# Optimization experiments

Measured on AMD Instinct MI355X. Metric: run time of the kernel, lower is better.

Reference implementation:

```python
import jax, jax.numpy as jnp
import numpy as np

TOTAL = 131072   # total frames across all utterances
SEG = 256        # number of utterances
FEAT = 78        # input feature dim (hardcoded by Linear(78,1024))
HID = 1024
NCLS = 10


def _linear_params(key, fan_in, fan_out):
    # torch nn.Linear default init: U(-1/sqrt(fan_in), 1/sqrt(fan_in))
    bound = 1.0 / np.sqrt(fan_in)
    kw, kb = jax.random.split(key)
    W = jax.random.uniform(kw, (fan_in, fan_out), minval=-bound, maxval=bound, dtype=jnp.float32)
    b = jax.random.uniform(kb, (fan_out,), minval=-bound, maxval=bound, dtype=jnp.float32)
    return W, b


def setup_inputs() -> dict:
    key = jax.random.key(0)
    ks = jax.random.split(key, 8)
    # ragged lengths summing exactly to TOTAL
    rng = np.random.default_rng(0)
    raw = rng.integers(256, 768, size=SEG).astype(np.float64)
    lens = np.maximum(1, (raw * TOTAL / raw.sum()).astype(np.int64))
    lens[-1] += TOTAL - lens.sum()
    lengths = jnp.asarray(lens, dtype=jnp.int32)

    x = jax.random.normal(ks[0], (TOTAL, FEAT), dtype=jnp.float32)
    W1, b1 = _linear_params(ks[1], FEAT, HID)
    W2, b2 = _linear_params(ks[2], HID, HID)
    W3, b3 = _linear_params(ks[3], HID, HID)
    W4, b4 = _linear_params(ks[4], HID, HID)
    W5, b5 = _linear_params(ks[5], HID, 1)
    W6, b6 = _linear_params(ks[6], HID, HID)
    W7, b7 = _linear_params(ks[7], HID, NCLS)
    return dict(x=x, W1=W1, b1=b1, W2=W2, b2=b2, W3=W3, b3=b3, W4=W4, b4=b4,
                W5=W5, b5=b5, W6=W6, b6=b6, W7=W7, b7=b7, lengths=lengths)


def reference(x, W1, b1, W2, b2, W3, b3, W4, b4, W5, b5, W6, b6, W7, b7, lengths):
    h = jax.nn.relu(x @ W1 + b1)
    h = jax.nn.relu(h @ W2 + b2)
    h = jax.nn.relu(h @ W3 + b3)
    h = jax.nn.relu(h @ W4 + b4)            # [N, HID]
    scores = jax.nn.relu(h @ W5 + b5)[:, 0]  # per-frame attention logit [N]

    # per-segment softmax over frames, then weighted sum pooling (fused segment ops)
    n_seg = lengths.shape[0]
    seg = jnp.repeat(jnp.arange(n_seg, dtype=jnp.int32), lengths,
                     total_repeat_length=h.shape[0])          # [N] segment ids
    m = jax.ops.segment_max(scores, seg, num_segments=n_seg)  # stable softmax max
    e = jnp.exp(scores - m[seg])
    denom = jax.ops.segment_sum(e, seg, num_segments=n_seg)
    w = e / denom[seg]                                        # [N] softmax weights
    pooled = jax.ops.segment_sum(h * w[:, None], seg, num_segments=n_seg)  # [SEG, HID]

    out = jax.nn.relu(pooled @ W6 + b6) @ W7 + b7             # [SEG, 10]
    return out
```

## Files before the change

### kernel.cpp

```cpp
#include <hip/hip_runtime.h>
#include <hip/hip_fp16.h>

#define TOTAL 131072
#define SEGN  256
#define FEAT  78
#define FPAD  96
#define HID   1024
#define NCLS  10
#define FCHUNK 32

typedef __attribute__((ext_vector_type(8))) short short8;
typedef __attribute__((ext_vector_type(4))) float floatx4;

typedef __attribute__((address_space(1))) void gvoid_t;
typedef __attribute__((address_space(3))) void svoid_t;

__device__ __forceinline__ void async_copy16(const void* gsrc, void* ldst) {
    __builtin_amdgcn_global_load_lds((gvoid_t*)(void*)gsrc, (svoid_t*)ldst, 16, 0, 0);
}


__global__ void conv_x_slab(const float* __restrict__ x, __half* __restrict__ xb,
                            int row0, int rows) {
    int idx = blockIdx.x * 256 + threadIdx.x;
    if (idx >= rows * FPAD) return;
    int col = idx % FPAD;
    int r   = idx / FPAD;
    float v = (col < FEAT) ? x[(size_t)(row0 + r) * FEAT + col] : 0.0f;
    xb[idx] = __float2half(v);
}

__global__ void conv_wt_kernel(const float* __restrict__ W, __half* __restrict__ Wt,
                               int K, int N, int Kpad) {
    int idx = blockIdx.x * 256 + threadIdx.x;
    if (idx >= N * Kpad) return;
    int k = idx % Kpad;
    int n = idx / Kpad;
    float v = (k < K) ? W[(size_t)k * N + n] : 0.0f;
    Wt[idx] = __float2half(v);
}

__global__ void conv_w4_kernel(const float* __restrict__ W2, const float* __restrict__ W3,
                               const float* __restrict__ W4, const float* __restrict__ W6,
                               __half* __restrict__ w2t, __half* __restrict__ w3t,
                               __half* __restrict__ w4t, __half* __restrict__ w6t) {
    int idx = blockIdx.x * 256 + threadIdx.x;
    if (idx >= HID * HID) return;
    int k = idx % HID;
    int n = idx / HID;
    const float* Ws[4] = {W2, W3, W4, W6};
    __half* Ts[4] = {w2t, w3t, w4t, w6t};
    int w = blockIdx.y;
    Ts[w][idx] = __float2half(Ws[w][(size_t)k * HID + n]);
}


__global__ __launch_bounds__(256, 2)
void gemm_f16(const __half* __restrict__ A, const __half* __restrict__ Bt,
              __half* __restrict__ C, const float* __restrict__ bias,
              int M, int N, int K, int relu_flag)
{
    __shared__ __align__(16) short smem[128 * 32 * 2];
    short* lds_a = smem;
    short* lds_b = smem + 128 * 32;

    const int t   = threadIdx.x;
    const int nbn = N >> 7;
    const int nbm = M >> 7;
    int bm, bn;
    {
        const int b = blockIdx.x;
        if ((nbm & 7) == 0) {
            const int xcd = b & 7;
            const int j   = b >> 3;
            bm = xcd * (nbm >> 3) + j / nbn;
            bn = j % nbn;
        } else {
            bn = b % nbn;
            bm = b / nbn;
        }
    }
    const size_t m0 = (size_t)bm * 128;
    const size_t n0 = (size_t)bn * 128;
    const int wave = t >> 6, lane = t & 63;
    const int wm = (wave >> 1) << 6;
    const int wn = (wave & 1) << 6;
    const int l16 = lane & 15, q = lane >> 4;

    floatx4 acc[4][4] = {};

    const int c0 = t, c1 = t + 256;
    const __half* a0 = A  + (m0 + (size_t)(c0 >> 2)) * K + (c0 & 3) * 8;
    const __half* a1 = A  + (m0 + (size_t)(c1 >> 2)) * K + (c1 & 3) * 8;
    const __half* b0 = Bt + (n0 + (size_t)(c0 >> 2)) * K + (c0 & 3) * 8;
    const __half* b1 = Bt + (n0 + (size_t)(c1 >> 2)) * K + (c1 & 3) * 8;
    short* la0 = &lds_a[c0 * 8];
    short* la1 = &lds_a[c1 * 8];
    short* lb0 = &lds_b[c0 * 8];
    short* lb1 = &lds_b[c1 * 8];

    for (int k0 = 0; k0 < K; k0 += 32) {
        __syncthreads();
        async_copy16(a0 + k0, la0);
        async_copy16(a1 + k0, la1);
        async_copy16(b0 + k0, lb0);
        async_copy16(b1 + k0, lb1);
        __syncthreads();

        short8 af[4], bf[4];
#pragma unroll
        for (int i = 0; i < 4; ++i)
            af[i] = *(const short8*)&lds_a[(wm + i * 16 + l16) * 32 + q * 8];
#pragma unroll
        for (int i = 0; i < 4; ++i)
            bf[i] = *(const short8*)&lds_b[(wn + i * 16 + l16) * 32 + q * 8];

#pragma unroll
        for (int mi = 0; mi < 4; ++mi)
#pragma unroll
            for (int ni = 0; ni < 4; ++ni)
                acc[mi][ni] = __builtin_amdgcn_mfma_f32_16x16x32_f16(
                    af[mi], bf[ni], acc[mi][ni], 0, 0, 0);
    }

    __half* ct = (__half*)smem;
#pragma unroll
    for (int h = 0; h < 2; ++h) {
        __syncthreads();
        if (wm == h * 64) {
#pragma unroll
            for (int ni = 0; ni < 4; ++ni) {
                const int col = wn + ni * 16 + l16;
                const float bv = bias[n0 + col];
#pragma unroll
                for (int mi = 0; mi < 4; ++mi) {
                    const int r0l = mi * 16 + q * 4;
#pragma unroll
                    for (int r = 0; r < 4; ++r) {
                        float v = acc[mi][ni][r] + bv;
                        if (relu_flag) v = fmaxf(v, 0.0f);
                        ct[(r0l + r) * 128 + col] = __float2half(v);
                    }
                }
            }
        }
        __syncthreads();
#pragma unroll
        for (int it = 0; it < 4; ++it) {
            const int chunk = it * 256 + t;
            const int row = chunk >> 4;
            const int off = (chunk & 15) * 8;
            *(short8*)&C[(m0 + h * 64 + row) * N + n0 + off] =
                *(const short8*)&ct[row * 128 + off];
        }
    }
}


__global__ void seg_offsets_kernel(const int* __restrict__ lengths, int* __restrict__ off) {
    if (blockIdx.x == 0 && threadIdx.x == 0) {
        int a = 0;
        off[0] = 0;
        for (int i = 0; i < SEGN; ++i) { a += lengths[i]; off[i + 1] = a; }
    }
}


__global__ __launch_bounds__(256)
void escore_kernel(const __half* __restrict__ h4, int slab_beg,
                   const float* __restrict__ W5, const float* __restrict__ b5,
                   float* __restrict__ earr)
{
    const int fl   = blockIdx.x * 4 + (threadIdx.x >> 6);
    const int lane = threadIdx.x & 63;
    const __half* row = h4 + (size_t)fl * HID + lane * 16;
    const float*  wv  = W5 + lane * 16;

    short8 r0 = *(const short8*)row;
    short8 r1 = *(const short8*)(row + 8);
    float s = 0.f;
#pragma unroll
    for (int j = 0; j < 8; ++j) s += __half2float(((const __half*)&r0)[j]) * wv[j];
#pragma unroll
    for (int j = 0; j < 8; ++j) s += __half2float(((const __half*)&r1)[j]) * wv[j + 8];
#pragma unroll
    for (int o = 32; o > 0; o >>= 1) s += __shfl_down(s, o);
    if (lane == 0)
        earr[slab_beg + fl] = __expf(fminf(fmaxf(s + b5[0], 0.0f), 80.0f));
}


__global__ __launch_bounds__(256)
void pool_accum_kernel(const __half* __restrict__ h4, int slab_beg,
                       const float* __restrict__ earr, const int* __restrict__ segoff,
                       float* __restrict__ pooled)
{
    const int c0 = blockIdx.y * 512 + threadIdx.x * 2;
    const int f0 = slab_beg + blockIdx.x * FCHUNK;
    const int fend = f0 + FCHUNK;

    int lo = 0, hi = SEGN - 1;
    while (lo < hi) {
        int mid = (lo + hi + 1) >> 1;
        if (segoff[mid] <= f0) lo = mid; else hi = mid - 1;
    }
    int s = lo;

    const __half* base = h4 + (size_t)(f0 - slab_beg) * HID + c0;
    int f = f0;
    while (f < fend) {
        int send = segoff[s + 1];
        if (send > fend) send = fend;
        float a0 = 0.f, a1 = 0.f;
        for (; f < send; ++f, base += HID) {
            float e = earr[f];
            float2 fv = __half22float2(*(const __half2*)base);
            a0 += e * fv.x;
            a1 += e * fv.y;
        }
        float* p = pooled + (size_t)s * HID + c0;
        atomicAdd(p, a0);
        atomicAdd(p + 1, a1);
        ++s;
    }
}


__global__ __launch_bounds__(256)
void finalize_pool_kernel(const float* __restrict__ pooled, const float* __restrict__ earr,
                          const int* __restrict__ segoff, __half* __restrict__ poolh)
{
    int s = blockIdx.x, t = threadIdx.x;
    int beg = segoff[s], end = segoff[s + 1];
    __shared__ float sh[4];
    float es = 0.f;
    for (int i = beg + t; i < end; i += 256) es += earr[i];
#pragma unroll
    for (int o = 32; o > 0; o >>= 1) es += __shfl_down(es, o);
    if ((t & 63) == 0) sh[t >> 6] = es;
    __syncthreads();
    float inv = 1.0f / (sh[0] + sh[1] + sh[2] + sh[3]);
    for (int j = t; j < HID; j += 256)
        poolh[(size_t)s * HID + j] = __float2half(pooled[(size_t)s * HID + j] * inv);
}


__global__ void final_kernel(const __half* __restrict__ z, const float* __restrict__ W7,
                             const float* __restrict__ b7, float* __restrict__ out) {
    int s = blockIdx.x, t = threadIdx.x;
    float loc[NCLS];
#pragma unroll
    for (int c = 0; c < NCLS; ++c) loc[c] = 0.f;
    for (int k = t; k < HID; k += 256) {
        float zk = __half2float(z[(size_t)s * HID + k]);
        const float* wr = W7 + k * NCLS;
#pragma unroll
        for (int c = 0; c < NCLS; ++c) loc[c] += zk * wr[c];
    }
#pragma unroll
    for (int c = 0; c < NCLS; ++c)
#pragma unroll
        for (int o = 32; o > 0; o >>= 1) loc[c] += __shfl_down(loc[c], o);
    __shared__ float accs[NCLS];
    if (t < NCLS) accs[t] = 0.f;
    __syncthreads();
    if ((t & 63) == 0)
        for (int c = 0; c < NCLS; ++c) atomicAdd(&accs[c], loc[c]);
    __syncthreads();
    if (t < NCLS) out[s * NCLS + t] = accs[t] + b7[t];
}


extern "C" void kernel_launch(void* const* d_in, const int* in_sizes, int n_in,
                              void* d_out, int out_size, void* d_ws, size_t ws_size,
                              hipStream_t stream) {
    const float* x  = (const float*)d_in[0];
    const float* W1 = (const float*)d_in[1];
    const float* b1 = (const float*)d_in[2];
    const float* W2 = (const float*)d_in[3];
    const float* b2 = (const float*)d_in[4];
    const float* W3 = (const float*)d_in[5];
    const float* b3 = (const float*)d_in[6];
    const float* W4 = (const float*)d_in[7];
    const float* b4 = (const float*)d_in[8];
    const float* W5 = (const float*)d_in[9];
    const float* b5 = (const float*)d_in[10];
    const float* W6 = (const float*)d_in[11];
    const float* b6 = (const float*)d_in[12];
    const float* W7 = (const float*)d_in[13];
    const float* b7 = (const float*)d_in[14];
    const int* lengths = (const int*)d_in[15];
    float* out = (float*)d_out;

    char* ws = (char*)d_ws;
    size_t off = 0;
    auto take = [&](size_t bytes) -> char* {
        char* p = ws + off;
        off = (off + bytes + 255) & ~(size_t)255;
        return p;
    };
    __half* w1t   = (__half*)take((size_t)HID * FPAD * 2);
    __half* w2t   = (__half*)take((size_t)HID * HID * 2);
    __half* w3t   = (__half*)take((size_t)HID * HID * 2);
    __half* w4t   = (__half*)take((size_t)HID * HID * 2);
    __half* w6t   = (__half*)take((size_t)HID * HID * 2);
    int*    segoff = (int*)take((SEGN + 1) * 4);
    float*  pooled = (float*)take((size_t)SEGN * HID * 4);
    __half* poolh  = (__half*)take((size_t)SEGN * HID * 2);
    __half* z      = (__half*)take((size_t)SEGN * HID * 2);
    float*  earr   = (float*)take((size_t)TOTAL * 4);

    int R = TOTAL;
    while (R > 1024) {
        size_t need = off + (size_t)R * FPAD * 2 + 2 * (size_t)R * HID * 2 + 3 * 256;
        if (need <= ws_size) break;
        R >>= 1;
    }
    __half* slabX = (__half*)take((size_t)R * FPAD * 2);
    __half* slabA = (__half*)take((size_t)R * HID * 2);
    __half* slabB = (__half*)take((size_t)R * HID * 2);

    seg_offsets_kernel<<<1, 64, 0, stream>>>(lengths, segoff);
    hipMemsetAsync(pooled, 0, (size_t)SEGN * HID * 4, stream);

    conv_wt_kernel<<<(HID * FPAD + 255) / 256, 256, 0, stream>>>(W1, w1t, FEAT, HID, FPAD);
    dim3 gW((HID * HID + 255) / 256, 4);
    conv_w4_kernel<<<gW, 256, 0, stream>>>(W2, W3, W4, W6, w2t, w3t, w4t, w6t);

    const int nBlocksSlab = (R / 128) * (HID / 128);
    dim3 gPool(R / FCHUNK, 2);
    for (int sb = 0; sb < TOTAL; sb += R) {
        conv_x_slab<<<(R * FPAD + 255) / 256, 256, 0, stream>>>(x, slabX, sb, R);
        gemm_f16<<<nBlocksSlab, 256, 0, stream>>>(slabX, w1t, slabA, b1, R, HID, FPAD, 1);
        gemm_f16<<<nBlocksSlab, 256, 0, stream>>>(slabA, w2t, slabB, b2, R, HID, HID, 1);
        gemm_f16<<<nBlocksSlab, 256, 0, stream>>>(slabB, w3t, slabA, b3, R, HID, HID, 1);
        gemm_f16<<<nBlocksSlab, 256, 0, stream>>>(slabA, w4t, slabB, b4, R, HID, HID, 1);
        escore_kernel<<<R / 4, 256, 0, stream>>>(slabB, sb, W5, b5, earr);
        pool_accum_kernel<<<gPool, 256, 0, stream>>>(slabB, sb, earr, segoff, pooled);
    }

    finalize_pool_kernel<<<SEGN, 256, 0, stream>>>(pooled, earr, segoff, poolh);
    const int nBlocksHead = (SEGN / 128) * (HID / 128);
    gemm_f16<<<nBlocksHead, 256, 0, stream>>>(poolh, w6t, z, b6, SEGN, HID, HID, 1);
    final_kernel<<<SEGN, 256, 0, stream>>>(z, W7, b7, out);
}
```

Before: 1.336 ms.

## Swizzle GEMM LDS layout, add single-shot K=96 GEMM, fuse scoring with pooling

Applies an XOR swizzle to the LDS tile layout in the main f16 GEMM so the MFMA fragment reads hit fewer bank conflicts. Adds a dedicated first-layer GEMM that loads the whole K=96 tile once instead of looping over K-steps with barriers. Fuses the attention-score kernel with the pooling kernel, so exp-scores stay in shared memory and the softmax denominator is accumulated atomically, removing the earr round trip and a separate reduction in finalize. The trade-off is more atomics on the denominator and more per-block work in the fused kernel.

```diff
diff --git a/kernel.cpp b/kernel.cpp
--- a/kernel.cpp
+++ b/kernel.cpp
@@ -18,6 +18,8 @@
 __device__ __forceinline__ void async_copy16(const void* gsrc, void* ldst) {
     __builtin_amdgcn_global_load_lds((gvoid_t*)(void*)gsrc, (svoid_t*)ldst, 16, 0, 0);
 }
+
+__device__ __forceinline__ int xswz(int r) { return (r & 3) ^ ((r >> 2) & 3); }
 
 
 __global__ void conv_x_slab(const float* __restrict__ x, __half* __restrict__ xb,
@@ -90,15 +92,20 @@
     floatx4 acc[4][4] = {};
 
     const int c0 = t, c1 = t + 256;
-    const __half* a0 = A  + (m0 + (size_t)(c0 >> 2)) * K + (c0 & 3) * 8;
-    const __half* a1 = A  + (m0 + (size_t)(c1 >> 2)) * K + (c1 & 3) * 8;
-    const __half* b0 = Bt + (n0 + (size_t)(c0 >> 2)) * K + (c0 & 3) * 8;
-    const __half* b1 = Bt + (n0 + (size_t)(c1 >> 2)) * K + (c1 & 3) * 8;
+    const int r0s = c0 >> 2, r1s = c1 >> 2;
+    const int g0 = (c0 & 3) ^ xswz(r0s);
+    const int g1 = (c1 & 3) ^ xswz(r1s);
+    const __half* a0 = A  + (m0 + (size_t)r0s) * K + g0 * 8;
+    const __half* a1 = A  + (m0 + (size_t)r1s) * K + g1 * 8;
+    const __half* b0 = Bt + (n0 + (size_t)r0s) * K + g0 * 8;
+    const __half* b1 = Bt + (n0 + (size_t)r1s) * K + g1 * 8;
     short* la0 = &lds_a[c0 * 8];
     short* la1 = &lds_a[c1 * 8];
     short* lb0 = &lds_b[c0 * 8];
     short* lb1 = &lds_b[c1 * 8];
 
+    const int xq = (q ^ (l16 & 3) ^ ((l16 >> 2) & 3)) * 8;
+
     for (int k0 = 0; k0 < K; k0 += 32) {
         __syncthreads();
         async_copy16(a0 + k0, la0);
@@ -110,10 +117,10 @@
         short8 af[4], bf[4];
 #pragma unroll
         for (int i = 0; i < 4; ++i)
-            af[i] = *(const short8*)&lds_a[(wm + i * 16 + l16) * 32 + q * 8];
+            af[i] = *(const short8*)&lds_a[(wm + i * 16 + l16) * 32 + xq];
 #pragma unroll
         for (int i = 0; i < 4; ++i)
-            bf[i] = *(const short8*)&lds_b[(wn + i * 16 + l16) * 32 + q * 8];
+            bf[i] = *(const short8*)&lds_b[(wn + i * 16 + l16) * 32 + xq];
 
 #pragma unroll
         for (int mi = 0; mi < 4; ++mi)
@@ -157,6 +164,100 @@
 }
 
 
+__global__ __launch_bounds__(256, 2)
+void gemm_k96(const __half* __restrict__ A, const __half* __restrict__ Bt,
+              __half* __restrict__ C, const float* __restrict__ bias, int M, int N)
+{
+    __shared__ __align__(16) short smem[2 * 128 * 96];
+    short* lds_a = smem;
+    short* lds_b = smem + 128 * 96;
+
+    const int t   = threadIdx.x;
+    const int nbn = N >> 7;
+    const int nbm = M >> 7;
+    int bm, bn;
+    {
+        const int b = blockIdx.x;
+        if ((nbm & 7) == 0) {
+            const int xcd = b & 7;
+            const int j   = b >> 3;
+            bm = xcd * (nbm >> 3) + j / nbn;
+            bn = j % nbn;
+        } else {
+            bn = b % nbn;
+            bm = b / nbn;
+        }
+    }
+    const size_t m0 = (size_t)bm * 128;
+    const size_t n0 = (size_t)bn * 128;
+    const int wave = t >> 6, lane = t & 63;
+    const int wm = (wave >> 1) << 6;
+    const int wn = (wave & 1) << 6;
+    const int l16 = lane & 15, q = lane >> 4;
+
+#pragma unroll
+    for (int i = 0; i < 6; ++i) {
+        const int c = i * 256 + t;
+        const int r = c / 12, j = c % 12;
+        const int g = (j >> 2) * 4 + ((j & 3) ^ xswz(r));
+        async_copy16(A  + (m0 + (size_t)r) * 96 + g * 8, &lds_a[c * 8]);
+        async_copy16(Bt + (n0 + (size_t)r) * 96 + g * 8, &lds_b[c * 8]);
+    }
+    __syncthreads();
+
+    floatx4 acc[4][4] = {};
+    const int xql = ((q ^ (l16 & 3) ^ ((l16 >> 2) & 3))) * 8;
+#pragma unroll
+    for (int ks = 0; ks < 3; ++ks) {
+        short8 af[4], bf[4];
+        const int xo = ks * 32 + xql;
+#pragma unroll
+        for (int i = 0; i < 4; ++i)
+            af[i] = *(const short8*)&lds_a[(wm + i * 16 + l16) * 96 + xo];
+#pragma unroll
+        for (int i = 0; i < 4; ++i)
+            bf[i] = *(const short8*)&lds_b[(wn + i * 16 + l16) * 96 + xo];
+#pragma unroll
+        for (int mi = 0; mi < 4; ++mi)
+#pragma unroll
+            for (int ni = 0; ni < 4; ++ni)
+                acc[mi][ni] = __builtin_amdgcn_mfma_f32_16x16x32_f16(
+                    af[mi], bf[ni], acc[mi][ni], 0, 0, 0);
+    }
+
+    __half* ct = (__half*)smem;
+#pragma unroll
+    for (int h = 0; h < 2; ++h) {
+        __syncthreads();
+        if (wm == h * 64) {
+#pragma unroll
+            for (int ni = 0; ni < 4; ++ni) {
+                const int col = wn + ni * 16 + l16;
+                const float bv = bias[n0 + col];
+#pragma unroll
+                for (int mi = 0; mi < 4; ++mi) {
+                    const int r0l = mi * 16 + q * 4;
+#pragma unroll
+                    for (int r = 0; r < 4; ++r) {
+                        float v = fmaxf(acc[mi][ni][r] + bv, 0.0f);
+                        ct[(r0l + r) * 128 + col] = __float2half(v);
+                    }
+                }
+            }
+        }
+        __syncthreads();
+#pragma unroll
+        for (int it = 0; it < 4; ++it) {
+            const int chunk = it * 256 + t;
+            const int row = chunk >> 4;
+            const int off = (chunk & 15) * 8;
+            *(short8*)&C[(m0 + h * 64 + row) * N + n0 + off] =
+                *(const short8*)&ct[row * 128 + off];
+        }
+    }
+}
+
+
 __global__ void seg_offsets_kernel(const int* __restrict__ lengths, int* __restrict__ off) {
     if (blockIdx.x == 0 && threadIdx.x == 0) {
         int a = 0;
@@ -167,79 +268,74 @@
 
 
 __global__ __launch_bounds__(256)
-void escore_kernel(const __half* __restrict__ h4, int slab_beg,
-                   const float* __restrict__ W5, const float* __restrict__ b5,
-                   float* __restrict__ earr)
+void scorepool_kernel(const __half* __restrict__ h4, int slab_beg,
+                      const float* __restrict__ W5, const float* __restrict__ b5,
+                      const int* __restrict__ segoff,
+                      float* __restrict__ pooled, float* __restrict__ denom)
 {
-    const int fl   = blockIdx.x * 4 + (threadIdx.x >> 6);
-    const int lane = threadIdx.x & 63;
-    const __half* row = h4 + (size_t)fl * HID + lane * 16;
-    const float*  wv  = W5 + lane * 16;
-
-    short8 r0 = *(const short8*)row;
-    short8 r1 = *(const short8*)(row + 8);
-    float s = 0.f;
-#pragma unroll
-    for (int j = 0; j < 8; ++j) s += __half2float(((const __half*)&r0)[j]) * wv[j];
-#pragma unroll
-    for (int j = 0; j < 8; ++j) s += __half2float(((const __half*)&r1)[j]) * wv[j + 8];
-#pragma unroll
-    for (int o = 32; o > 0; o >>= 1) s += __shfl_down(s, o);
-    if (lane == 0)
-        earr[slab_beg + fl] = __expf(fminf(fmaxf(s + b5[0], 0.0f), 80.0f));
-}
-
-
-__global__ __launch_bounds__(256)
-void pool_accum_kernel(const __half* __restrict__ h4, int slab_beg,
-                       const float* __restrict__ earr, const int* __restrict__ segoff,
-                       float* __restrict__ pooled)
-{
-    const int c0 = blockIdx.y * 512 + threadIdx.x * 2;
+    __shared__ float e_sh[FCHUNK];
+    const int t = threadIdx.x, wave = t >> 6, lane = t & 63;
     const int f0 = slab_beg + blockIdx.x * FCHUNK;
-    const int fend = f0 + FCHUNK;
-
+    const float b5v = b5[0];
+
+#pragma unroll
+    for (int i = 0; i < 8; ++i) {
+        const int fl = wave * 8 + i;
+        const __half* row = h4 + (size_t)(f0 - slab_beg + fl) * HID + lane * 16;
+        const float* wv = W5 + lane * 16;
+        short8 r0 = *(const short8*)row;
+        short8 r1 = *(const short8*)(row + 8);
+        float s = 0.f;
+#pragma unroll
+        for (int j = 0; j < 8; ++j) s += __half2float(((const __half*)&r0)[j]) * wv[j];
+#pragma unroll
+        for (int j = 0; j < 8; ++j) s += __half2float(((const __half*)&r1)[j]) * wv[j + 8];
+#pragma unroll
+        for (int o = 32; o > 0; o >>= 1) s += __shfl_down(s, o);
+        if (lane == 0)
+            e_sh[fl] = __expf(fminf(fmaxf(s + b5v, 0.0f), 80.0f));
+    }
+    __syncthreads();
+
+    const int c0 = t * 4;
     int lo = 0, hi = SEGN - 1;
     while (lo < hi) {
         int mid = (lo + hi + 1) >> 1;
         if (segoff[mid] <= f0) lo = mid; else hi = mid - 1;
     }
     int s = lo;
-
+    int f = f0;
+    const int fend = f0 + FCHUNK;
     const __half* base = h4 + (size_t)(f0 - slab_beg) * HID + c0;
-    int f = f0;
     while (f < fend) {
         int send = segoff[s + 1];
         if (send > fend) send = fend;
-        float a0 = 0.f, a1 = 0.f;
+        float a0 = 0.f, a1 = 0.f, a2 = 0.f, a3 = 0.f, es = 0.f;
         for (; f < send; ++f, base += HID) {
-            float e = earr[f];
-            float2 fv = __half22float2(*(const __half2*)base);
-            a0 += e * fv.x;
-            a1 += e * fv.y;
+            float e = e_sh[f - f0];
+            const __half2* r2 = (const __half2*)base;
+            float2 u = __half22float2(r2[0]);
+            float2 v = __half22float2(r2[1]);
+            a0 += e * u.x; a1 += e * u.y; a2 += e * v.x; a3 += e * v.y;
+            es += e;
         }
         float* p = pooled + (size_t)s * HID + c0;
-        atomicAdd(p, a0);
+        atomicAdd(p,     a0);
         atomicAdd(p + 1, a1);
+        atomicAdd(p + 2, a2);
+        atomicAdd(p + 3, a3);
+        if (t == 0) atomicAdd(&denom[s], es);
         ++s;
     }
 }
 
 
 __global__ __launch_bounds__(256)
-void finalize_pool_kernel(const float* __restrict__ pooled, const float* __restrict__ earr,
-                          const int* __restrict__ segoff, __half* __restrict__ poolh)
+void finalize_pool_kernel(const float* __restrict__ pooled, const float* __restrict__ denom,
+                          __half* __restrict__ poolh)
 {
     int s = blockIdx.x, t = threadIdx.x;
-    int beg = segoff[s], end = segoff[s + 1];
-    __shared__ float sh[4];
-    float es = 0.f;
-    for (int i = beg + t; i < end; i += 256) es += earr[i];
-#pragma unroll
-    for (int o = 32; o > 0; o >>= 1) es += __shfl_down(es, o);
-    if ((t & 63) == 0) sh[t >> 6] = es;
-    __syncthreads();
-    float inv = 1.0f / (sh[0] + sh[1] + sh[2] + sh[3]);
+    float inv = 1.0f / denom[s];
     for (int j = t; j < HID; j += 256)
         poolh[(size_t)s * HID + j] = __float2half(pooled[(size_t)s * HID + j] * inv);
 }
@@ -306,9 +402,9 @@
     __half* w6t   = (__half*)take((size_t)HID * HID * 2);
     int*    segoff = (int*)take((SEGN + 1) * 4);
     float*  pooled = (float*)take((size_t)SEGN * HID * 4);
+    float*  denom  = (float*)take(SEGN * 4);
     __half* poolh  = (__half*)take((size_t)SEGN * HID * 2);
     __half* z      = (__half*)take((size_t)SEGN * HID * 2);
-    float*  earr   = (float*)take((size_t)TOTAL * 4);
 
     int R = TOTAL;
     while (R > 1024) {
@@ -322,24 +418,23 @@
 
     seg_offsets_kernel<<<1, 64, 0, stream>>>(lengths, segoff);
     hipMemsetAsync(pooled, 0, (size_t)SEGN * HID * 4, stream);
+    hipMemsetAsync(denom, 0, SEGN * 4, stream);
 
     conv_wt_kernel<<<(HID * FPAD + 255) / 256, 256, 0, stream>>>(W1, w1t, FEAT, HID, FPAD);
     dim3 gW((HID * HID + 255) / 256, 4);
     conv_w4_kernel<<<gW, 256, 0, stream>>>(W2, W3, W4, W6, w2t, w3t, w4t, w6t);
 
     const int nBlocksSlab = (R / 128) * (HID / 128);
-    dim3 gPool(R / FCHUNK, 2);
     for (int sb = 0; sb < TOTAL; sb += R) {
         conv_x_slab<<<(R * FPAD + 255) / 256, 256, 0, stream>>>(x, slabX, sb, R);
-        gemm_f16<<<nBlocksSlab, 256, 0, stream>>>(slabX, w1t, slabA, b1, R, HID, FPAD, 1);
+        gemm_k96<<<nBlocksSlab, 256, 0, stream>>>(slabX, w1t, slabA, b1, R, HID);
         gemm_f16<<<nBlocksSlab, 256, 0, stream>>>(slabA, w2t, slabB, b2, R, HID, HID, 1);
         gemm_f16<<<nBlocksSlab, 256, 0, stream>>>(slabB, w3t, slabA, b3, R, HID, HID, 1);
         gemm_f16<<<nBlocksSlab, 256, 0, stream>>>(slabA, w4t, slabB, b4, R, HID, HID, 1);
-        escore_kernel<<<R / 4, 256, 0, stream>>>(slabB, sb, W5, b5, earr);
-        pool_accum_kernel<<<gPool, 256, 0, stream>>>(slabB, sb, earr, segoff, pooled);
-    }
-
-    finalize_pool_kernel<<<SEGN, 256, 0, stream>>>(pooled, earr, segoff, poolh);
+        scorepool_kernel<<<R / FCHUNK, 256, 0, stream>>>(slabB, sb, W5, b5, segoff, pooled, denom);
+    }
+
+    finalize_pool_kernel<<<SEGN, 256, 0, stream>>>(pooled, denom, poolh);
     const int nBlocksHead = (SEGN / 128) * (HID / 128);
     gemm_f16<<<nBlocksHead, 256, 0, stream>>>(poolh, w6t, z, b6, SEGN, HID, HID, 1);
     final_kernel<<<SEGN, 256, 0, stream>>>(z, W7, b7, out);
```

Measured after the change: 1.369 ms. +2.5%, slower.
